# Optimization experiments

Hardware: AMD Instinct MI355X
Metric: run time of the kernel (lower is better)

The kernel has to match this reference:

```python
import jax, jax.numpy as jnp
import numpy as np

P = 8        # patch (window) size
HEADS = 6
E = 192
HD = E // HEADS


def _layernorm(x, g, b, eps=1e-5):
    m = x.mean(-1, keepdims=True)
    v = ((x - m) ** 2).mean(-1, keepdims=True)
    return (x - m) / jnp.sqrt(v + eps) * g + b


def setup_inputs() -> dict:
    key = jax.random.key(0)
    ks = jax.random.split(key, 8)
    B, H, W = 8, 128, 128
    return {
        "x": jax.random.normal(ks[0], (B, E, H, W), jnp.float32),
        "row_embed": jax.random.uniform(ks[1], (P, E // 2), jnp.float32),
        "col_embed": jax.random.uniform(ks[2], (P, E // 2), jnp.float32),
        "ln1_g": jnp.ones((E,), jnp.float32),
        "ln1_b": jnp.zeros((E,), jnp.float32),
        "in_proj_w": jax.random.normal(ks[3], (3 * E, E), jnp.float32) * 0.02,
        "in_proj_b": jnp.zeros((3 * E,), jnp.float32),
        "out_w": jax.random.normal(ks[4], (E, E), jnp.float32) * 0.02,
        "out_b": jnp.zeros((E,), jnp.float32),
        "ln2_g": jnp.ones((E,), jnp.float32),
        "ln2_b": jnp.zeros((E,), jnp.float32),
        "ffn_w1": jax.random.normal(ks[5], (4 * E, E), jnp.float32) * 0.02,
        "ffn_b1": jnp.zeros((4 * E,), jnp.float32),
        "ffn_w2": jax.random.normal(ks[6], (E, 4 * E), jnp.float32) * 0.02,
        "ffn_b2": jnp.zeros((E,), jnp.float32),
    }


def reference(x, row_embed, col_embed, ln1_g, ln1_b, in_proj_w, in_proj_b,
              out_w, out_b, ln2_g, ln2_b, ffn_w1, ffn_b1, ffn_w2, ffn_b2):
    B, C, H, W = x.shape
    hp, wp = H // P, W // P
    # shift_size=0 and H,W multiples of P -> no roll, no padding, no mask.
    # to_patches: 'b c (hp p1) (wp p2) -> (p1 p2) (b hp wp) c'
    xp = (x.reshape(B, C, hp, P, wp, P)
           .transpose(3, 5, 0, 2, 4, 1)          # (p1, p2, B, hp, wp, C)
           .reshape(P * P, B * hp * wp, C))      # (L, N, C)
    # learnable positional embedding: (p^2, 1, E)
    pos = jnp.concatenate(
        [jnp.repeat(row_embed[:, None, :], P, axis=1),
         jnp.repeat(col_embed[None, :, :], P, axis=0)], axis=-1
    ).reshape(P * P, 1, C)
    xp = xp + pos
    residual = xp
    xn = _layernorm(xp, ln1_g, ln1_b)
    # self-attention (q = k = v = xn), torch MultiheadAttention math
    qkv = xn @ in_proj_w.T + in_proj_b            # (L, N, 3E)
    q, k, v = jnp.split(qkv, 3, axis=-1)
    L, N, _ = q.shape
    q = q.reshape(L, N, HEADS, HD)
    k = k.reshape(L, N, HEADS, HD)
    v = v.reshape(L, N, HEADS, HD)
    scale = 1.0 / jnp.sqrt(jnp.asarray(HD, jnp.float32))
    scores = jnp.einsum('lnhd,mnhd->nhlm', q * scale, k)   # (N, H, L, L)
    attn = jax.nn.softmax(scores, axis=-1)
    o = jnp.einsum('nhlm,mnhd->lnhd', attn, v).reshape(L, N, C)
    o = o @ out_w.T + out_b
    xp = o + residual
    # FFN (note: GELU after BOTH linears, per the source)
    h = _layernorm(xp, ln2_g, ln2_b)
    h = jax.nn.gelu(h @ ffn_w1.T + ffn_b1, approximate=False)
    h = jax.nn.gelu(h @ ffn_w2.T + ffn_b2, approximate=False)
    xp = xp + h
    # reverse rearrange: '(p1 p2) (b hp wp) c -> b c (hp p1) (wp p2)'
    out = (xp.reshape(P, P, B, hp, wp, C)
             .transpose(2, 5, 3, 0, 4, 1)        # (B, C, hp, p1, wp, p2)
             .reshape(B, C, H, W))
    return out
```

## Files before the change

### kernel.cpp

```cpp
#include <hip/hip_runtime.h>
#include <hip/hip_bf16.h>

typedef unsigned short u16;
typedef __bf16 bf16x8 __attribute__((ext_vector_type(8)));
typedef float f32x4 __attribute__((ext_vector_type(4)));

__device__ __forceinline__ u16 f2b(float f) {
  __hip_bfloat16 h = __float2bfloat16(f);
  return *reinterpret_cast<u16*>(&h);
}
__device__ __forceinline__ float b2f(u16 v) {
  unsigned int u = ((unsigned int)v) << 16;
  union { unsigned int u; float f; } c; c.u = u; return c.f;
}
__device__ __forceinline__ float gelu_f(float x) {
  float t = x * x;
  float u = x * fmaf(t, -0.10294576f, -2.30220813f);
  float e = exp2f(u);
  return x * __builtin_amdgcn_rcpf(1.0f + e);
}

__global__ __launch_bounds__(256) void k_cvt(const float* __restrict__ s, u16* __restrict__ d, int n) {
  int i = blockIdx.x * 256 + threadIdx.x;
  if (i < n) d[i] = f2b(s[i]);
}

__global__ __launch_bounds__(256) void k_patchify_ln(const float* __restrict__ x,
                                                     const float* __restrict__ rowe,
                                                     const float* __restrict__ cole,
                                                     const float* __restrict__ g,
                                                     const float* __restrict__ bta,
                                                     u16* __restrict__ resid,
                                                     u16* __restrict__ xn, int b0) {
  __shared__ float tile[192 * 133];
  __shared__ float ps[256], pq[256], mb[128], rb[128];
  const int h = blockIdx.x, bb = blockIdx.y, b = b0 + bb;
  const int tid = threadIdx.x;
  const int p1 = h & 7, hy = h >> 3;
  const float* xs = x + ((size_t)b * 192 * 128 + (size_t)h) * 128;
  for (int i = 0; i < 24; i++) {
    int idx = i * 256 + tid;
    int c = idx >> 5, w4 = idx & 31;
    const float4 v = *reinterpret_cast<const float4*>(xs + (size_t)c * 16384 + w4 * 4);
    float a0, a1, a2, a3;
    if (c < 96) {
      float pv = rowe[p1 * 96 + c];
      a0 = a1 = a2 = a3 = pv;
    } else {
      int w = w4 * 4;
      a0 = cole[((w)     & 7) * 96 + c - 96];
      a1 = cole[((w + 1) & 7) * 96 + c - 96];
      a2 = cole[((w + 2) & 7) * 96 + c - 96];
      a3 = cole[((w + 3) & 7) * 96 + c - 96];
    }
    float* t = &tile[c * 133 + w4 * 4];
    t[0] = v.x + a0; t[1] = v.y + a1; t[2] = v.z + a2; t[3] = v.w + a3;
  }
  __syncthreads();
  {
    int w = tid & 127, half = tid >> 7;
    float s = 0.f, q = 0.f;
    for (int c = half * 96; c < half * 96 + 96; c++) {
      float v = tile[c * 133 + w];
      s += v; q += v * v;
    }
    ps[tid] = s; pq[tid] = q;
  }
  __syncthreads();
  if (tid < 128) {
    float s = ps[tid] + ps[tid + 128];
    float q = pq[tid] + pq[tid + 128];
    float mean = s * (1.f / 192.f);
    float var = q * (1.f / 192.f) - mean * mean;
    mb[tid] = mean;
    rb[tid] = rsqrtf(var + 1e-5f);
  }
  __syncthreads();
  for (int i = 0; i < 96; i++) {
    int idx = i * 256 + tid;
    int w = idx / 192, c = idx - w * 192;
    float v = tile[c * 133 + w];
    int wx = w >> 3, p2 = w & 7;
    size_t rr = ((size_t)((bb * 16 + hy) * 16 + wx)) * 64 + p1 * 8 + p2;
    resid[rr * 192 + c] = f2b(v);
    xn[rr * 192 + c] = f2b((v - mb[w]) * rb[w] * g[c] + bta[c]);
  }
}

enum { EP_BF16 = 0, EP_GELU_BF16 = 1, EP_GELU_ADD = 3 };

template <int BN, int EP, int KTOT>
__global__ __launch_bounds__(256, 2) void k_gemm3(const u16* __restrict__ A,
                                                  const u16* __restrict__ W,
                                                  const float* __restrict__ bias,
                                                  const void* __restrict__ aux,
                                                  void* __restrict__ outp, int Nout) {
  constexpr int NF = BN / 32;
  constexpr int NBS = BN / 32;
  constexpr int NK = KTOT / 64;
  __shared__ __align__(16) u16 ldsA[2][128 * 64];
  __shared__ __align__(16) u16 ldsB[2][BN * 64];
  const int tid = threadIdx.x;
  const int lane = tid & 63, wid = tid >> 6;
  const int lo = lane & 15, hi = lane >> 4;
  const int wm = wid >> 1, wn = wid & 1;
  const int n0 = blockIdx.x * BN;
  const int m0 = blockIdx.y * 128;

  const int lrow = lane >> 3, lk = (lane & 7) * 8;
  const u16* agp[4];
  const u16* bgp[NBS];
#pragma unroll
  for (int i = 0; i < 4; i++)
    agp[i] = A + (size_t)(m0 + i * 32 + wid * 8 + lrow) * KTOT + lk;
#pragma unroll
  for (int i = 0; i < NBS; i++)
    bgp[i] = W + (size_t)(n0 + i * 32 + wid * 8 + lrow) * KTOT + lk;

  auto stage = [&](int kc, int buf) {
#pragma unroll
    for (int i = 0; i < 4; i++)
      __builtin_amdgcn_global_load_lds(
          (const __attribute__((address_space(1))) void*)(agp[i] + kc * 64),
          (__attribute__((address_space(3))) void*)(&ldsA[buf][(i * 4 + wid) * 512]), 16, 0, 0);
#pragma unroll
    for (int i = 0; i < NBS; i++)
      __builtin_amdgcn_global_load_lds(
          (const __attribute__((address_space(1))) void*)(bgp[i] + kc * 64),
          (__attribute__((address_space(3))) void*)(&ldsB[buf][(i * 4 + wid) * 512]), 16, 0, 0);
  };

  f32x4 acc[4][NF] = {};
  stage(0, 0);
  __syncthreads();
  for (int kc = 0; kc < NK; kc++) {
    if (kc + 1 < NK) stage(kc + 1, (kc + 1) & 1);
    const u16* bufA = ldsA[kc & 1];
    const u16* bufB = ldsB[kc & 1];
#pragma unroll
    for (int kt = 0; kt < 2; kt++) {
      bf16x8 a[4], b[NF];
#pragma unroll
      for (int mi = 0; mi < 4; mi++)
        a[mi] = *reinterpret_cast<const bf16x8*>(&bufA[(wm * 64 + mi * 16 + lo) * 64 + kt * 32 + hi * 8]);
#pragma unroll
      for (int nj = 0; nj < NF; nj++)
        b[nj] = *reinterpret_cast<const bf16x8*>(&bufB[(wn * (BN / 2) + nj * 16 + lo) * 64 + kt * 32 + hi * 8]);
#pragma unroll
      for (int mi = 0; mi < 4; mi++)
#pragma unroll
        for (int nj = 0; nj < NF; nj++)
          acc[mi][nj] = __builtin_amdgcn_mfma_f32_16x16x32_bf16(a[mi], b[nj], acc[mi][nj], 0, 0, 0);
    }
    __syncthreads();
  }
#pragma unroll
  for (int mi = 0; mi < 4; mi++)
#pragma unroll
    for (int nj = 0; nj < NF; nj++) {
      int gn = n0 + wn * (BN / 2) + nj * 16 + lo;
      float bv = bias[gn];
#pragma unroll
      for (int r = 0; r < 4; r++) {
        int gm = m0 + wm * 64 + mi * 16 + hi * 4 + r;
        size_t oidx = (size_t)gm * Nout + gn;
        float v = acc[mi][nj][r] + bv;
        if (EP == EP_BF16)           ((u16*)outp)[oidx] = f2b(v);
        else if (EP == EP_GELU_BF16) ((u16*)outp)[oidx] = f2b(gelu_f(v));
        else                         ((float*)outp)[oidx] = gelu_f(v) + b2f(((const u16*)aux)[oidx]);
      }
    }
}

__global__ __launch_bounds__(256, 2) void k_oproj_ln(const u16* __restrict__ A,
                                                     const u16* __restrict__ W,
                                                     const float* __restrict__ bias,
                                                     const u16* __restrict__ resid,
                                                     const float* __restrict__ g,
                                                     const float* __restrict__ bt,
                                                     u16* __restrict__ xp2,
                                                     u16* __restrict__ xn) {
  __shared__ __align__(16) u16 ldsA[2][128 * 64];
  __shared__ __align__(16) u16 ldsB[2][192 * 64];
  const int tid = threadIdx.x;
  const int lane = tid & 63, wid = tid >> 6;
  const int lo = lane & 15, hi = lane >> 4;
  const int wm = wid >> 1, wn = wid & 1;
  const size_t m0 = (size_t)blockIdx.x * 128;
  const int lrow = lane >> 3, lk = (lane & 7) * 8;

  auto stage = [&](int kc, int buf) {
#pragma unroll
    for (int i = 0; i < 4; i++)
      __builtin_amdgcn_global_load_lds(
          (const __attribute__((address_space(1))) void*)(A + (m0 + i * 32 + wid * 8 + lrow) * 192 + kc * 64 + lk),
          (__attribute__((address_space(3))) void*)(&ldsA[buf][(i * 4 + wid) * 512]), 16, 0, 0);
#pragma unroll
    for (int i = 0; i < 6; i++)
      __builtin_amdgcn_global_load_lds(
          (const __attribute__((address_space(1))) void*)(W + (size_t)(i * 32 + wid * 8 + lrow) * 192 + kc * 64 + lk),
          (__attribute__((address_space(3))) void*)(&ldsB[buf][(i * 4 + wid) * 512]), 16, 0, 0);
  };

  f32x4 acc[4][6] = {};
  stage(0, 0);
  __syncthreads();
  for (int kc = 0; kc < 3; kc++) {
    if (kc + 1 < 3) stage(kc + 1, (kc + 1) & 1);
    const u16* bufA = ldsA[kc & 1];
    const u16* bufB = ldsB[kc & 1];
#pragma unroll
    for (int kt = 0; kt < 2; kt++) {
      bf16x8 a[4], b[6];
#pragma unroll
      for (int mi = 0; mi < 4; mi++)
        a[mi] = *reinterpret_cast<const bf16x8*>(&bufA[(wm * 64 + mi * 16 + lo) * 64 + kt * 32 + hi * 8]);
#pragma unroll
      for (int nj = 0; nj < 6; nj++)
        b[nj] = *reinterpret_cast<const bf16x8*>(&bufB[(wn * 96 + nj * 16 + lo) * 64 + kt * 32 + hi * 8]);
#pragma unroll
      for (int mi = 0; mi < 4; mi++)
#pragma unroll
        for (int nj = 0; nj < 6; nj++)
          acc[mi][nj] = __builtin_amdgcn_mfma_f32_16x16x32_bf16(a[mi], b[nj], acc[mi][nj], 0, 0, 0);
    }
    __syncthreads();
  }
  float bv[6];
#pragma unroll
  for (int nj = 0; nj < 6; nj++) bv[nj] = bias[wn * 96 + nj * 16 + lo];
#pragma unroll
  for (int mi = 0; mi < 4; mi++)
#pragma unroll
    for (int r = 0; r < 4; r++) {
      size_t gm = m0 + wm * 64 + mi * 16 + hi * 4 + r;
#pragma unroll
      for (int nj = 0; nj < 6; nj++)
        acc[mi][nj][r] += bv[nj] + b2f(resid[gm * 192 + wn * 96 + nj * 16 + lo]);
    }
  float* scr_s = (float*)&ldsA[0][0];
  float* scr_q = scr_s + 256;
#pragma unroll
  for (int mi = 0; mi < 4; mi++)
#pragma unroll
    for (int r = 0; r < 4; r++) {
      float s = 0.f, q = 0.f;
#pragma unroll
      for (int nj = 0; nj < 6; nj++) { float v = acc[mi][nj][r]; s += v; q += v * v; }
      s += __shfl_xor(s, 1, 64); q += __shfl_xor(q, 1, 64);
      s += __shfl_xor(s, 2, 64); q += __shfl_xor(q, 2, 64);
      s += __shfl_xor(s, 4, 64); q += __shfl_xor(q, 4, 64);
      s += __shfl_xor(s, 8, 64); q += __shfl_xor(q, 8, 64);
      if (lo == 0) {
        int row = wm * 64 + mi * 16 + hi * 4 + r;
        scr_s[row * 2 + wn] = s;
        scr_q[row * 2 + wn] = q;
      }
    }
  __syncthreads();
#pragma unroll
  for (int mi = 0; mi < 4; mi++)
#pragma unroll
    for (int r = 0; r < 4; r++) {
      int row = wm * 64 + mi * 16 + hi * 4 + r;
      float s = scr_s[row * 2] + scr_s[row * 2 + 1];
      float q = scr_q[row * 2] + scr_q[row * 2 + 1];
      float mean = s * (1.f / 192.f);
      float rstd = rsqrtf(q * (1.f / 192.f) - mean * mean + 1e-5f);
#pragma unroll
      for (int nj = 0; nj < 6; nj++) {
        int gn = wn * 96 + nj * 16 + lo;
        size_t oidx = (m0 + row) * 192 + gn;
        float v = acc[mi][nj][r];
        xp2[oidx] = f2b(v);
        xn[oidx] = f2b((v - mean) * rstd * g[gn] + bt[gn]);
      }
    }
}

__global__ __launch_bounds__(384, 3) void k_attn2(const u16* __restrict__ qkv, u16* __restrict__ o) {
  __shared__ __align__(16) u16 vt[192 * 72];
  __shared__ __align__(16) u16 pbuf[6 * 64 * 64];
  const int tid = threadIdx.x;
  const int wid = tid >> 6, lane = tid & 63, lo = lane & 15, hi = lane >> 4;
  const u16* src = qkv + (size_t)blockIdx.x * 64 * 576;
  for (int i = 0; i < 4; i++) {
    int gq = i * 384 + tid, row = gq / 24, kk = gq - row * 24;
    uint4 d = *reinterpret_cast<const uint4*>(src + row * 576 + 384 + kk * 8);
    const u16* ds = (const u16*)&d;
#pragma unroll
    for (int e = 0; e < 8; e++) vt[(kk * 8 + e) * 72 + row] = ds[e];
  }
  bf16x8 qa[4], kb[4];
#pragma unroll
  for (int mi = 0; mi < 4; mi++)
    qa[mi] = *reinterpret_cast<const bf16x8*>(src + (size_t)(mi * 16 + lo) * 576 + wid * 32 + hi * 8);
#pragma unroll
  for (int nj = 0; nj < 4; nj++)
    kb[nj] = *reinterpret_cast<const bf16x8*>(src + (size_t)(nj * 16 + lo) * 576 + 192 + wid * 32 + hi * 8);
  f32x4 s[4][4] = {};
#pragma unroll
  for (int mi = 0; mi < 4; mi++)
#pragma unroll
    for (int nj = 0; nj < 4; nj++)
      s[mi][nj] = __builtin_amdgcn_mfma_f32_16x16x32_bf16(qa[mi], kb[nj], s[mi][nj], 0, 0, 0);
  const float scale = 0.1767766952966369f;
#pragma unroll
  for (int mi = 0; mi < 4; mi++)
#pragma unroll
    for (int nj = 0; nj < 4; nj++)
#pragma unroll
      for (int r = 0; r < 4; r++) s[mi][nj][r] *= scale;
  const int l3 = lo & 7, lh = lo >> 3;
#pragma unroll
  for (int mi = 0; mi < 4; mi++)
#pragma unroll
    for (int r = 0; r < 4; r++) {
      float mx = fmaxf(fmaxf(s[mi][0][r], s[mi][1][r]), fmaxf(s[mi][2][r], s[mi][3][r]));
      mx = fmaxf(mx, __shfl_xor(mx, 1, 64));
      mx = fmaxf(mx, __shfl_xor(mx, 2, 64));
      mx = fmaxf(mx, __shfl_xor(mx, 4, 64));
      mx = fmaxf(mx, __shfl_xor(mx, 8, 64));
      float e0 = __expf(s[mi][0][r] - mx), e1 = __expf(s[mi][1][r] - mx);
      float e2 = __expf(s[mi][2][r] - mx), e3 = __expf(s[mi][3][r] - mx);
      float sm = e0 + e1 + e2 + e3;
      sm += __shfl_xor(sm, 1, 64);
      sm += __shfl_xor(sm, 2, 64);
      sm += __shfl_xor(sm, 4, 64);
      sm += __shfl_xor(sm, 8, 64);
      float inv = 1.0f / sm;
      int ii = mi * 16 + hi * 4 + r;
      u16* bse = pbuf + wid * 4096 + ii * 64;
      int x7 = ii & 7;
      bse[((lh)     ^ x7) * 8 + l3] = f2b(e0 * inv);
      bse[((2 + lh) ^ x7) * 8 + l3] = f2b(e1 * inv);
      bse[((4 + lh) ^ x7) * 8 + l3] = f2b(e2 * inv);
      bse[((6 + lh) ^ x7) * 8 + l3] = f2b(e3 * inv);
    }
  __syncthreads();
  f32x4 oacc[4][2] = {};
#pragma unroll
  for (int kt = 0; kt < 2; kt++) {
    bf16x8 pa[4], vb[2];
#pragma unroll
    for (int mi = 0; mi < 4; mi++) {
      int row = mi * 16 + lo;
      pa[mi] = *reinterpret_cast<const bf16x8*>(pbuf + wid * 4096 + row * 64 + ((kt * 4 + hi) ^ (row & 7)) * 8);
    }
#pragma unroll
    for (int ni = 0; ni < 2; ni++)
      vb[ni] = *reinterpret_cast<const bf16x8*>(vt + (wid * 32 + ni * 16 + lo) * 72 + kt * 32 + hi * 8);
#pragma unroll
    for (int mi = 0; mi < 4; mi++)
#pragma unroll
      for (int ni = 0; ni < 2; ni++)
        oacc[mi][ni] = __builtin_amdgcn_mfma_f32_16x16x32_bf16(pa[mi], vb[ni], oacc[mi][ni], 0, 0, 0);
  }
#pragma unroll
  for (int mi = 0; mi < 4; mi++)
#pragma unroll
    for (int ni = 0; ni < 2; ni++)
#pragma unroll
      for (int r = 0; r < 4; r++) {
        int i = mi * 16 + hi * 4 + r, d = ni * 16 + lo;
        o[((size_t)blockIdx.x * 64 + i) * 192 + wid * 32 + d] = f2b(oacc[mi][ni][r]);
      }
}

__global__ __launch_bounds__(256) void k_unpatch(const float* __restrict__ xf, float* __restrict__ outp, int b0) {
  __shared__ float tile[128 * 65];
  const int cc = blockIdx.x, h = blockIdx.y, bb = blockIdx.z, b = b0 + bb;
  const int tid = threadIdx.x;
  const int p1 = h & 7, hy = h >> 3;
  for (int i = 0; i < 32; i++) {
    int idx = i * 256 + tid, t = idx >> 6, c = idx & 63;
    int wx = t >> 3, p2 = t & 7;
    int rr = ((bb * 16 + hy) * 16 + wx) * 64 + p1 * 8 + p2;
    tile[t * 65 + c] = xf[(size_t)rr * 192 + cc * 64 + c];
  }
  __syncthreads();
  for (int i = 0; i < 32; i++) {
    int idx = i * 256 + tid, c = idx >> 7, w = idx & 127;
    outp[((size_t)(b * 192 + cc * 64 + c) * 128 + h) * 128 + w] = tile[w * 65 + c];
  }
}

extern "C" void kernel_launch(void* const* d_in, const int* in_sizes, int n_in,
                              void* d_out, int out_size, void* d_ws, size_t ws_size,
                              hipStream_t stream) {
  const float* x    = (const float*)d_in[0];
  const float* rowe = (const float*)d_in[1];
  const float* cole = (const float*)d_in[2];
  const float* ln1g = (const float*)d_in[3];
  const float* ln1b = (const float*)d_in[4];
  const float* ipw  = (const float*)d_in[5];
  const float* ipb  = (const float*)d_in[6];
  const float* outw = (const float*)d_in[7];
  const float* outb = (const float*)d_in[8];
  const float* ln2g = (const float*)d_in[9];
  const float* ln2b = (const float*)d_in[10];
  const float* w1   = (const float*)d_in[11];
  const float* b1   = (const float*)d_in[12];
  const float* w2   = (const float*)d_in[13];
  const float* b2   = (const float*)d_in[14];
  float* outp = (float*)d_out;

  char* p = (char*)d_ws;
  auto alloc = [&](size_t bytes) -> void* {
    void* r = (void*)p;
    p += (bytes + 255) & ~(size_t)255;
    return r;
  };
  u16* wq  = (u16*)alloc(110592 * 2);
  u16* wo  = (u16*)alloc(36864 * 2);
  u16* wf1 = (u16*)alloc(147456 * 2);
  u16* wf2 = (u16*)alloc(147456 * 2);

  size_t used = (size_t)(p - (char*)d_ws);
  size_t avail = (ws_size > used) ? (ws_size - used) : 0;
  int NC = 1;
  while (NC < 8 && (size_t)(131072 / NC) * 3840 + 8192 > avail) NC *= 2;
  const int Bc = 8 / NC;
  const size_t Mc = (size_t)Bc * 16384;

  u16*   resid = (u16*)alloc(Mc * 192 * 2);
  u16*   xn    = (u16*)alloc(Mc * 192 * 2);
  u16*   big   = (u16*)alloc(Mc * 768 * 2);
  u16*   obuf  = (u16*)alloc(Mc * 192 * 2);
  u16*   xp2   = (u16*)alloc(Mc * 192 * 2);
  float* xfin  = (float*)alloc(Mc * 192 * 4);

  k_cvt<<<dim3((110592 + 255) / 256), dim3(256), 0, stream>>>(ipw, wq, 110592);
  k_cvt<<<dim3((36864 + 255) / 256), dim3(256), 0, stream>>>(outw, wo, 36864);
  k_cvt<<<dim3((147456 + 255) / 256), dim3(256), 0, stream>>>(w1, wf1, 147456);
  k_cvt<<<dim3((147456 + 255) / 256), dim3(256), 0, stream>>>(w2, wf2, 147456);

  for (int ch = 0; ch < NC; ch++) {
    int b0 = ch * Bc;
    k_patchify_ln<<<dim3(128, Bc), dim3(256), 0, stream>>>(x, rowe, cole, ln1g, ln1b, resid, xn, b0);
    k_gemm3<96, EP_BF16, 192><<<dim3(6, (unsigned)(Mc / 128)), dim3(256), 0, stream>>>(xn, wq, ipb, nullptr, big, 576);
    k_attn2<<<dim3((unsigned)(Bc * 256)), dim3(384), 0, stream>>>(big, obuf);
    k_oproj_ln<<<dim3((unsigned)(Mc / 128)), dim3(256), 0, stream>>>(obuf, wo, outb, resid, ln2g, ln2b, xp2, xn);
    k_gemm3<128, EP_GELU_BF16, 192><<<dim3(6, (unsigned)(Mc / 128)), dim3(256), 0, stream>>>(xn, wf1, b1, nullptr, big, 768);
    k_gemm3<96, EP_GELU_ADD, 768><<<dim3(2, (unsigned)(Mc / 128)), dim3(256), 0, stream>>>(big, wf2, b2, xp2, xfin, 192);
    k_unpatch<<<dim3(3, 128, Bc), dim3(256), 0, stream>>>(xfin, outp, b0);
  }
}
```

Baseline: 705.9 us.

## Fuse FFN2 GEMM epilogue with unpatch transpose, drop fp32 intermediate buffer

Adds a dedicated FFN2 GEMM kernel whose epilogue applies GELU and the residual add, transposes the tile through LDS, and writes directly into the NCHW output with float4 stores. This removes the separate unpatch kernel and the fp32 xfin buffer, so one full fp32 write and read of the activations goes away. Dropping that buffer also shrinks the per-chunk workspace, which may allow fewer chunks. The LDS is reused for the transpose after the main loop.

```diff
diff --git a/kernel.cpp b/kernel.cpp
--- a/kernel.cpp
+++ b/kernel.cpp
@@ -87,13 +87,12 @@
   }
 }
 
-enum { EP_BF16 = 0, EP_GELU_BF16 = 1, EP_GELU_ADD = 3 };
+enum { EP_BF16 = 0, EP_GELU_BF16 = 1 };
 
 template <int BN, int EP, int KTOT>
 __global__ __launch_bounds__(256, 2) void k_gemm3(const u16* __restrict__ A,
                                                   const u16* __restrict__ W,
                                                   const float* __restrict__ bias,
-                                                  const void* __restrict__ aux,
                                                   void* __restrict__ outp, int Nout) {
   constexpr int NF = BN / 32;
   constexpr int NBS = BN / 32;
@@ -165,11 +164,100 @@
         int gm = m0 + wm * 64 + mi * 16 + hi * 4 + r;
         size_t oidx = (size_t)gm * Nout + gn;
         float v = acc[mi][nj][r] + bv;
-        if (EP == EP_BF16)           ((u16*)outp)[oidx] = f2b(v);
-        else if (EP == EP_GELU_BF16) ((u16*)outp)[oidx] = f2b(gelu_f(v));
-        else                         ((float*)outp)[oidx] = gelu_f(v) + b2f(((const u16*)aux)[oidx]);
+        if (EP == EP_BF16) ((u16*)outp)[oidx] = f2b(v);
+        else               ((u16*)outp)[oidx] = f2b(gelu_f(v));
       }
     }
+}
+
+__global__ __launch_bounds__(256, 2) void k_ffn2_up(const u16* __restrict__ A,
+                                                    const u16* __restrict__ W,
+                                                    const float* __restrict__ bias,
+                                                    const u16* __restrict__ xp2,
+                                                    float* __restrict__ outp, int b0) {
+  __shared__ __align__(16) u16 smem[2 * 128 * 64 + 2 * 96 * 64];
+  u16* ldsA = smem;
+  u16* ldsB = smem + 2 * 128 * 64;
+  float* trans = (float*)smem;
+  const int tid = threadIdx.x;
+  const int lane = tid & 63, wid = tid >> 6;
+  const int lo = lane & 15, hi = lane >> 4;
+  const int wm = wid >> 1, wn = wid & 1;
+  const int n0 = blockIdx.x * 96;
+  const size_t m0 = (size_t)blockIdx.y * 128;
+  const int lrow = lane >> 3, lk = (lane & 7) * 8;
+
+  auto stage = [&](int kc, int buf) {
+#pragma unroll
+    for (int i = 0; i < 4; i++)
+      __builtin_amdgcn_global_load_lds(
+          (const __attribute__((address_space(1))) void*)(A + (m0 + i * 32 + wid * 8 + lrow) * 768 + kc * 64 + lk),
+          (__attribute__((address_space(3))) void*)(ldsA + buf * 8192 + (i * 4 + wid) * 512), 16, 0, 0);
+#pragma unroll
+    for (int i = 0; i < 3; i++)
+      __builtin_amdgcn_global_load_lds(
+          (const __attribute__((address_space(1))) void*)(W + (size_t)(n0 + i * 32 + wid * 8 + lrow) * 768 + kc * 64 + lk),
+          (__attribute__((address_space(3))) void*)(ldsB + buf * 6144 + (i * 4 + wid) * 512), 16, 0, 0);
+  };
+
+  f32x4 acc[4][3] = {};
+  stage(0, 0);
+  __syncthreads();
+  for (int kc = 0; kc < 12; kc++) {
+    if (kc + 1 < 12) stage(kc + 1, (kc + 1) & 1);
+    const u16* bufA = ldsA + (kc & 1) * 8192;
+    const u16* bufB = ldsB + (kc & 1) * 6144;
+#pragma unroll
+    for (int kt = 0; kt < 2; kt++) {
+      bf16x8 a[4], b[3];
+#pragma unroll
+      for (int mi = 0; mi < 4; mi++)
+        a[mi] = *reinterpret_cast<const bf16x8*>(&bufA[(wm * 64 + mi * 16 + lo) * 64 + kt * 32 + hi * 8]);
+#pragma unroll
+      for (int nj = 0; nj < 3; nj++)
+        b[nj] = *reinterpret_cast<const bf16x8*>(&bufB[(wn * 48 + nj * 16 + lo) * 64 + kt * 32 + hi * 8]);
+#pragma unroll
+      for (int mi = 0; mi < 4; mi++)
+#pragma unroll
+        for (int nj = 0; nj < 3; nj++)
+          acc[mi][nj] = __builtin_amdgcn_mfma_f32_16x16x32_bf16(a[mi], b[nj], acc[mi][nj], 0, 0, 0);
+    }
+    __syncthreads();
+  }
+  float bv[3];
+#pragma unroll
+  for (int nj = 0; nj < 3; nj++) bv[nj] = bias[n0 + wn * 48 + nj * 16 + lo];
+#pragma unroll
+  for (int mi = 0; mi < 4; mi++)
+#pragma unroll
+    for (int nj = 0; nj < 3; nj++) {
+      int cl = wn * 48 + nj * 16 + lo;
+#pragma unroll
+      for (int r = 0; r < 4; r++) {
+        int px = wm * 64 + mi * 16 + hi * 4 + r;
+        float v = gelu_f(acc[mi][nj][r] + bv[nj]) + b2f(xp2[(m0 + px) * 192 + n0 + cl]);
+        trans[cl * 129 + px] = v;
+      }
+    }
+  __syncthreads();
+#pragma unroll
+  for (int j = 0; j < 12; j++) {
+    int q = j * 256 + tid;
+    int c = q >> 5;
+    int wq = q & 31;
+    int px = wq * 4;
+    float v0 = trans[c * 129 + px];
+    float v1 = trans[c * 129 + px + 1];
+    float v2 = trans[c * 129 + px + 2];
+    float v3 = trans[c * 129 + px + 3];
+    int tok = (int)m0 + px;
+    int wnd = tok >> 6, p = tok & 63;
+    int p1 = p >> 3, p2 = p & 7;
+    int bb = wnd >> 8, hy = (wnd >> 4) & 15, wx = wnd & 15;
+    size_t o = (((size_t)((b0 + bb) * 192 + n0 + c) * 128) + hy * 8 + p1) * 128 + wx * 8 + p2;
+    float4 v = make_float4(v0, v1, v2, v3);
+    *reinterpret_cast<float4*>(outp + o) = v;
+  }
 }
 
 __global__ __launch_bounds__(256, 2) void k_oproj_ln(const u16* __restrict__ A,
@@ -367,24 +455,6 @@
       }
 }
 
-__global__ __launch_bounds__(256) void k_unpatch(const float* __restrict__ xf, float* __restrict__ outp, int b0) {
-  __shared__ float tile[128 * 65];
-  const int cc = blockIdx.x, h = blockIdx.y, bb = blockIdx.z, b = b0 + bb;
-  const int tid = threadIdx.x;
-  const int p1 = h & 7, hy = h >> 3;
-  for (int i = 0; i < 32; i++) {
-    int idx = i * 256 + tid, t = idx >> 6, c = idx & 63;
-    int wx = t >> 3, p2 = t & 7;
-    int rr = ((bb * 16 + hy) * 16 + wx) * 64 + p1 * 8 + p2;
-    tile[t * 65 + c] = xf[(size_t)rr * 192 + cc * 64 + c];
-  }
-  __syncthreads();
-  for (int i = 0; i < 32; i++) {
-    int idx = i * 256 + tid, c = idx >> 7, w = idx & 127;
-    outp[((size_t)(b * 192 + cc * 64 + c) * 128 + h) * 128 + w] = tile[w * 65 + c];
-  }
-}
-
 extern "C" void kernel_launch(void* const* d_in, const int* in_sizes, int n_in,
                               void* d_out, int out_size, void* d_ws, size_t ws_size,
                               hipStream_t stream) {
@@ -419,16 +489,15 @@
   size_t used = (size_t)(p - (char*)d_ws);
   size_t avail = (ws_size > used) ? (ws_size - used) : 0;
   int NC = 1;
-  while (NC < 8 && (size_t)(131072 / NC) * 3840 + 8192 > avail) NC *= 2;
+  while (NC < 8 && (size_t)(131072 / NC) * 3072 + 8192 > avail) NC *= 2;
   const int Bc = 8 / NC;
   const size_t Mc = (size_t)Bc * 16384;
 
-  u16*   resid = (u16*)alloc(Mc * 192 * 2);
-  u16*   xn    = (u16*)alloc(Mc * 192 * 2);
-  u16*   big   = (u16*)alloc(Mc * 768 * 2);
-  u16*   obuf  = (u16*)alloc(Mc * 192 * 2);
-  u16*   xp2   = (u16*)alloc(Mc * 192 * 2);
-  float* xfin  = (float*)alloc(Mc * 192 * 4);
+  u16* resid = (u16*)alloc(Mc * 192 * 2);
+  u16* xn    = (u16*)alloc(Mc * 192 * 2);
+  u16* big   = (u16*)alloc(Mc * 768 * 2);
+  u16* obuf  = (u16*)alloc(Mc * 192 * 2);
+  u16* xp2   = (u16*)alloc(Mc * 192 * 2);
 
   k_cvt<<<dim3((110592 + 255) / 256), dim3(256), 0, stream>>>(ipw, wq, 110592);
   k_cvt<<<dim3((36864 + 255) / 256), dim3(256), 0, stream>>>(outw, wo, 36864);
@@ -438,11 +507,10 @@
   for (int ch = 0; ch < NC; ch++) {
     int b0 = ch * Bc;
     k_patchify_ln<<<dim3(128, Bc), dim3(256), 0, stream>>>(x, rowe, cole, ln1g, ln1b, resid, xn, b0);
-    k_gemm3<96, EP_BF16, 192><<<dim3(6, (unsigned)(Mc / 128)), dim3(256), 0, stream>>>(xn, wq, ipb, nullptr, big, 576);
+    k_gemm3<96, EP_BF16, 192><<<dim3(6, (unsigned)(Mc / 128)), dim3(256), 0, stream>>>(xn, wq, ipb, big, 576);
     k_attn2<<<dim3((unsigned)(Bc * 256)), dim3(384), 0, stream>>>(big, obuf);
     k_oproj_ln<<<dim3((unsigned)(Mc / 128)), dim3(256), 0, stream>>>(obuf, wo, outb, resid, ln2g, ln2b, xp2, xn);
-    k_gemm3<128, EP_GELU_BF16, 192><<<dim3(6, (unsigned)(Mc / 128)), dim3(256), 0, stream>>>(xn, wf1, b1, nullptr, big, 768);
-    k_gemm3<96, EP_GELU_ADD, 768><<<dim3(2, (unsigned)(Mc / 128)), dim3(256), 0, stream>>>(big, wf2, b2, xp2, xfin, 192);
-    k_unpatch<<<dim3(3, 128, Bc), dim3(256), 0, stream>>>(xfin, outp, b0);
-  }
-}
+    k_gemm3<128, EP_GELU_BF16, 192><<<dim3(6, (unsigned)(Mc / 128)), dim3(256), 0, stream>>>(xn, wf1, b1, big, 768);
+    k_ffn2_up<<<dim3(2, (unsigned)(Mc / 128)), dim3(256), 0, stream>>>(big, wf2, b2, xp2, outp, b0);
+  }
+}
```

Measured after the change: 660.4 us. 1.07x faster.
